# Kernel tuning notes

Hardware: AMD Instinct MI355X
Metric: run time of the kernel (lower is better)

## Reference

```python
import jax, jax.numpy as jnp
import numpy as np
import math

B, T, D = 8, 512, 512
H_HEADS, DQ, DV = 8, 64, 64
N_LAYERS, D_HID = 6, 2048
VOCAB, N_CLASSES = 32000, 5
LN_EPS = 1e-5


def setup_inputs() -> dict:
    key = jax.random.key(0)
    ks = jax.random.split(key, 20)
    s = 0.02
    x = jax.random.randint(ks[0], (B, T), 0, VOCAB - 1)
    emb = jax.random.normal(ks[1], (VOCAB, D), jnp.float32) * s
    emb = emb.at[VOCAB - 1].set(0.0)  # padding_idx row is zero
    # per-layer params stacked on leading N axis; weights stored [in, out]
    Wq = jax.random.normal(ks[2], (N_LAYERS, D, H_HEADS * DQ), jnp.float32) * s
    bq = jnp.zeros((N_LAYERS, H_HEADS * DQ), jnp.float32)
    Wk = jax.random.normal(ks[3], (N_LAYERS, D, H_HEADS * DQ), jnp.float32) * s
    bk = jnp.zeros((N_LAYERS, H_HEADS * DQ), jnp.float32)
    Wv = jax.random.normal(ks[4], (N_LAYERS, D, H_HEADS * DV), jnp.float32) * s
    bv = jnp.zeros((N_LAYERS, H_HEADS * DV), jnp.float32)
    Wo = jax.random.normal(ks[5], (N_LAYERS, H_HEADS * DV, D), jnp.float32) * s
    bo = jnp.zeros((N_LAYERS, D), jnp.float32)
    gamma = jnp.ones((N_LAYERS, D), jnp.float32)
    beta = jnp.zeros((N_LAYERS, D), jnp.float32)
    W1 = jax.random.normal(ks[6], (N_LAYERS, D, D_HID), jnp.float32) * s
    b1 = jnp.zeros((N_LAYERS, D_HID), jnp.float32)
    W2 = jax.random.normal(ks[7], (N_LAYERS, D_HID, D), jnp.float32) * s
    b2 = jnp.zeros((N_LAYERS, D), jnp.float32)
    Wout = jax.random.normal(ks[8], (D * T, N_CLASSES), jnp.float32) * s
    bout = jnp.zeros((N_CLASSES,), jnp.float32)
    return dict(x=x, stage=0, emb=emb, Wq=Wq, bq=bq, Wk=Wk, bk=bk, Wv=Wv, bv=bv,
                Wo=Wo, bo=bo, gamma=gamma, beta=beta, W1=W1, b1=b1, W2=W2, b2=b2,
                Wout=Wout, bout=bout)


def _sinusoidal_pe(t, d):
    pos = jnp.arange(t, dtype=jnp.float32)[:, None]              # [T,1]
    inv = jnp.exp(jnp.arange(0, d, 2, dtype=jnp.float32) * (-math.log(10000.0) / d))
    ang = pos * inv[None, :]                                     # [T, D/2]
    pe = jnp.ones((t, d), jnp.float32)
    pe = pe.at[:, 0::2].set(jnp.sin(ang)).at[:, 1::2].set(jnp.cos(ang))
    return pe


def _layer_norm(x, g, b):
    mu = jnp.mean(x, -1, keepdims=True)
    var = jnp.mean((x - mu) ** 2, -1, keepdims=True)
    return g * (x - mu) * jax.lax.rsqrt(var + LN_EPS) + b


def _attn(x, wq, bq_, wk, bk_, wv, bv_, wo, bo_):
    b, t, _ = x.shape
    q = (x @ wq + bq_).reshape(b, t, H_HEADS, DQ).transpose(0, 2, 1, 3)  # [B,h,T,dq]
    k = (x @ wk + bk_).reshape(b, t, H_HEADS, DQ).transpose(0, 2, 1, 3)
    v = (x @ wv + bv_).reshape(b, t, H_HEADS, DV).transpose(0, 2, 1, 3)
    score = jnp.einsum('bhtd,bhsd->bhts', q, k)  # NOTE: no 1/sqrt(d) scaling, per source
    a = jax.nn.softmax(score, axis=-1)
    o = jnp.einsum('bhts,bhsv->bhtv', a, v)
    o = o.transpose(0, 2, 1, 3).reshape(b, t, H_HEADS * DV)
    return o @ wo + bo_


def reference(x, stage, emb, Wq, bq, Wk, bk, Wv, bv, Wo, bo, gamma, beta, W1, b1, W2, b2, Wout, bout):
    h = emb[x]                                   # [B,T,D]
    h = h + _sinusoidal_pe(h.shape[1], h.shape[2])[None]
    for i in range(N_LAYERS):
        res = h
        a = _attn(h, Wq[i], bq[i], Wk[i], bk[i], Wv[i], bv[i], Wo[i], bo[i])
        h = _layer_norm(a + res, gamma[i], beta[i])
        res = h
        f = jax.nn.relu(h @ W1[i] + b1[i]) @ W2[i] + b2[i]
        h = _layer_norm(f + res, gamma[i], beta[i])  # same LN params reused, per source
    out = h.reshape(h.shape[0], -1) @ Wout + bout
    return out
```

## Files before the change

### kernel.cpp

```cpp
#include <hip/hip_runtime.h>
#include <hip/hip_bf16.h>


typedef _Float16 f16_t;
typedef _Float16 f16x8 __attribute__((ext_vector_type(8)));
typedef _Float16 f16x4 __attribute__((ext_vector_type(4)));
typedef _Float16 f16x2 __attribute__((ext_vector_type(2)));
typedef float    f32x4 __attribute__((ext_vector_type(4)));

#define LSTR 3145728LL

__device__ __forceinline__ void gl_lds16(const f16_t* g, f16_t* l) {
    __builtin_amdgcn_global_load_lds(
        (const __attribute__((address_space(1))) unsigned int*)g,
        (__attribute__((address_space(3))) unsigned int*)l, 16, 0, 0);
}

template<int BM, int BN, int BK, int WR, int WC, int OUTF16, int RELU, int VOUT>
__global__ void __launch_bounds__(256)
gemm_kernel(const f16_t* __restrict__ A, const f16_t* __restrict__ B,
            const float* __restrict__ bias, void* __restrict__ Cout,
            f16_t* __restrict__ vt,
            int M, int N, int K, int lda, int ldb, int ldc, int zmod,
            long long sAhi, long long sAlo, long long sBhi, long long sBlo,
            long long sChi, long long sClo)
{
    constexpr int WMT = BM / WR;
    constexpr int WNT = BN / WC;
    constexpr int MR  = WMT / 16;
    constexpr int NR  = WNT / 16;
    constexpr int KK  = BK / 32;
    constexpr int CPR = BK / 8;
    constexpr int RS  = (BK == 32) ? 1 : 0;
    constexpr int IA  = BM * BK / 2048;
    constexpr int IB  = BN * BK / 2048;
    __shared__ __align__(16) f16_t As[2][BM][BK];
    __shared__ __align__(16) f16_t Bs[2][BN][BK];

    const int tid  = threadIdx.x;
    const int wid  = tid >> 6, lane = tid & 63;
    const int wr   = wid / WC, wc = wid % WC;
    const int z    = blockIdx.z;
    const int zh   = z / zmod, zl = z % zmod;
    const f16_t* Ab = A + (long long)zh * sAhi + (long long)zl * sAlo;
    const f16_t* Bb = B + (long long)zh * sBhi + (long long)zl * sBlo;
    const int m0 = blockIdx.x * BM;
    const int n0 = blockIdx.y * BN;

    f32x4 acc[MR][NR] = {};

    const f16_t* srcA[IA]; const f16_t* srcB[IB];
#pragma unroll
    for (int i = 0; i < IA; ++i) {
        const int c = i * 256 + tid, row = c / CPR;
        const int kch = (c % CPR) ^ ((row >> RS) & (CPR - 1));
        srcA[i] = Ab + (long long)(m0 + row) * lda + kch * 8;
    }
#pragma unroll
    for (int i = 0; i < IB; ++i) {
        const int c = i * 256 + tid, row = c / CPR;
        const int kch = (c % CPR) ^ ((row >> RS) & (CPR - 1));
        srcB[i] = Bb + (long long)(n0 + row) * ldb + kch * 8;
    }
    auto stage = [&](int bf_, int t) {
        const int k0 = t * BK;
#pragma unroll
        for (int i = 0; i < IA; ++i)
            gl_lds16(srcA[i] + k0, &As[bf_][0][0] + (i * 256 + wid * 64) * 8);
#pragma unroll
        for (int i = 0; i < IB; ++i)
            gl_lds16(srcB[i] + k0, &Bs[bf_][0][0] + (i * 256 + wid * 64) * 8);
    };

    const int l15 = lane & 15;
    const int g   = lane >> 4;
    int aoff[MR][KK], boff[NR][KK];
#pragma unroll
    for (int m = 0; m < MR; ++m) {
        const int row = wr * WMT + m * 16 + l15;
        const int swz = ((row >> RS) & (CPR - 1)) << 4;
#pragma unroll
        for (int kk = 0; kk < KK; ++kk)
            aoff[m][kk] = ((row * BK + kk * 32 + g * 8) * 2) ^ swz;
    }
#pragma unroll
    for (int n = 0; n < NR; ++n) {
        const int row = wc * WNT + n * 16 + l15;
        const int swz = ((row >> RS) & (CPR - 1)) << 4;
#pragma unroll
        for (int kk = 0; kk < KK; ++kk)
            boff[n][kk] = ((row * BK + kk * 32 + g * 8) * 2) ^ swz;
    }

    const int NT = K / BK;
    stage(0, 0);
    __syncthreads();

    int buf = 0;
    for (int t = 0; t < NT; ++t) {
        if (t + 1 < NT) stage(buf ^ 1, t + 1);
        const char* Al = (const char*)&As[buf][0][0];
        const char* Bl = (const char*)&Bs[buf][0][0];
        f16x8 af[MR][KK], bfr[NR][KK];
#pragma unroll
        for (int m = 0; m < MR; ++m)
#pragma unroll
            for (int kk = 0; kk < KK; ++kk) af[m][kk] = *(const f16x8*)(Al + aoff[m][kk]);
#pragma unroll
        for (int n = 0; n < NR; ++n)
#pragma unroll
            for (int kk = 0; kk < KK; ++kk) bfr[n][kk] = *(const f16x8*)(Bl + boff[n][kk]);
#pragma unroll
        for (int kk = 0; kk < KK; ++kk)
#pragma unroll
            for (int m = 0; m < MR; ++m)
#pragma unroll
                for (int n = 0; n < NR; ++n)
                    acc[m][n] = __builtin_amdgcn_mfma_f32_16x16x32_f16(af[m][kk], bfr[n][kk], acc[m][n], 0, 0, 0);
        __syncthreads();
        buf ^= 1;
    }

    const long long cOff = (long long)zh * sChi + (long long)zl * sClo;
    const int rbase = (lane >> 4) * 4;
#pragma unroll
    for (int m = 0; m < MR; ++m) {
        const int row = m0 + wr * WMT + m * 16 + rbase;
#pragma unroll
        for (int n = 0; n < NR; ++n) {
            const int col = n0 + wc * WNT + n * 16 + l15;
            const float bb = bias ? bias[col] : 0.0f;
            if (VOUT && col >= 1024) {
                const int hh = (col - 1024) >> 6, dv = (col - 1024) & 63;
                const int bb_ = row >> 9, t0 = row & 511;
                f16x4 v4;
#pragma unroll
                for (int r = 0; r < 4; ++r) v4[r] = (f16_t)(acc[m][n][r] + bb);
                *(f16x4*)&vt[((long long)((bb_ * 8 + hh) * 64 + dv)) * 512 + t0] = v4;
            } else {
#pragma unroll
                for (int r = 0; r < 4; ++r) {
                    float v = acc[m][n][r] + bb;
                    if (RELU) v = fmaxf(v, 0.0f);
                    const long long idx = cOff + (long long)(row + r) * ldc + col;
                    if (OUTF16) ((f16_t*)Cout)[idx] = (f16_t)v;
                    else        ((float*)Cout)[idx] = v;
                }
            }
        }
    }
}

__global__ void __launch_bounds__(256)
attn_flash_kernel(const f16_t* __restrict__ qkv, const f16_t* __restrict__ Vt,
                  f16_t* __restrict__ ao)
{
    __shared__ __align__(16) f16_t Ks[512 * 64];
    __shared__ __align__(16) f16_t Qs[64 * 64];
    __shared__ __align__(16) f16_t Ps[4][16 * 64];
    const int tid = threadIdx.x, wid = tid >> 6, lane = tid & 63;
    const int l15 = lane & 15, g = lane >> 4;
    const int z = blockIdx.y, b = z >> 3, hh = z & 7;
    const int q0 = blockIdx.x * 64;
    const f16_t* Kbase = qkv + (long long)b * 512 * 1536 + 512 + hh * 64;
    const f16_t* Qbase = qkv + (long long)(b * 512 + q0) * 1536 + hh * 64;
    const f16_t* Vbase = Vt + (long long)z * 32768;

#pragma unroll
    for (int i = 0; i < 16; ++i) {
        const int c = i * 256 + tid, t = c >> 3, j = c & 7;
        gl_lds16(Kbase + (long long)t * 1536 + ((j ^ (t & 7)) << 3), Ks + c * 8);
    }
#pragma unroll
    for (int i = 0; i < 2; ++i) {
        const int c = i * 256 + tid, t = c >> 3, j = c & 7;
        gl_lds16(Qbase + (long long)t * 1536 + ((j ^ (t & 7)) << 3), Qs + c * 8);
    }
    __syncthreads();

    const int q = wid * 16 + l15;
    f16x8 qf[2];
#pragma unroll
    for (int k = 0; k < 2; ++k)
        qf[k] = *(const f16x8*)(Qs + q * 64 + (((k * 4 + g) ^ (l15 & 7)) << 3));

    f32x4 ov[4] = {};
    float m_run = -1e30f, l_run = 0.0f;
    f16_t* Pw = &Ps[wid][0];

    for (int ck = 0; ck < 8; ++ck) {
        const int kc0 = ck * 64;
        f16x8 vf[4][2];
#pragma unroll
        for (int n = 0; n < 4; ++n)
#pragma unroll
            for (int k = 0; k < 2; ++k)
                vf[n][k] = *(const f16x8*)(Vbase + (n * 16 + l15) * 512 + kc0 + k * 32 + g * 8);
        f32x4 s[4] = {};
        __builtin_amdgcn_s_setprio(1);
#pragma unroll
        for (int k = 0; k < 2; ++k)
#pragma unroll
            for (int m = 0; m < 4; ++m) {
                const int key = kc0 + m * 16 + l15;
                const f16x8 a = *(const f16x8*)(Ks + key * 64 + (((k * 4 + g) ^ (key & 7)) << 3));
                s[m] = __builtin_amdgcn_mfma_f32_16x16x32_f16(a, qf[k], s[m], 0, 0, 0);
            }
        __builtin_amdgcn_s_setprio(0);
        float cmax = -1e30f;
#pragma unroll
        for (int m = 0; m < 4; ++m)
#pragma unroll
            for (int r = 0; r < 4; ++r) cmax = fmaxf(cmax, s[m][r]);
        cmax = fmaxf(cmax, __shfl_xor(cmax, 16, 64));
        cmax = fmaxf(cmax, __shfl_xor(cmax, 32, 64));
        const float mnew = fmaxf(m_run, cmax);
        const float corr = __expf(m_run - mnew);
        float csum = 0.0f;
#pragma unroll
        for (int m = 0; m < 4; ++m) {
            f16x4 p4;
#pragma unroll
            for (int r = 0; r < 4; ++r) {
                const float pe = __expf(s[m][r] - mnew);
                csum += pe;
                p4[r] = (f16_t)pe;
            }
            *(f16x4*)(Pw + l15 * 64 + ((((m * 2 + (g >> 1)) ^ (l15 & 7))) << 3) + ((g & 1) << 2)) = p4;
        }
        csum += __shfl_xor(csum, 16, 64);
        csum += __shfl_xor(csum, 32, 64);
        l_run = l_run * corr + csum;
        m_run = mnew;
        float cr[4];
#pragma unroll
        for (int r = 0; r < 4; ++r) cr[r] = __shfl(corr, g * 4 + r, 64);
#pragma unroll
        for (int n = 0; n < 4; ++n)
#pragma unroll
            for (int r = 0; r < 4; ++r) ov[n][r] *= cr[r];
#pragma unroll
        for (int k = 0; k < 2; ++k) {
            const f16x8 pf = *(const f16x8*)(Pw + l15 * 64 + (((k * 4 + g) ^ (l15 & 7)) << 3));
            __builtin_amdgcn_s_setprio(1);
#pragma unroll
            for (int n = 0; n < 4; ++n)
                ov[n] = __builtin_amdgcn_mfma_f32_16x16x32_f16(pf, vf[n][k], ov[n], 0, 0, 0);
            __builtin_amdgcn_s_setprio(0);
        }
    }

    const float inv = 1.0f / l_run;
    float ir[4];
#pragma unroll
    for (int r = 0; r < 4; ++r) ir[r] = __shfl(inv, g * 4 + r, 64);
#pragma unroll
    for (int n = 0; n < 4; ++n)
#pragma unroll
        for (int r = 0; r < 4; ++r) {
            const long long row = b * 512 + q0 + wid * 16 + g * 4 + r;
            ao[row * 512 + hh * 64 + n * 16 + l15] = (f16_t)(ov[n][r] * ir[r]);
        }
}

__global__ void __launch_bounds__(256)
setup_kernel(const float* __restrict__ Wq, const float* __restrict__ Wk,
             const float* __restrict__ Wv, const float* __restrict__ Wo,
             const float* __restrict__ W1, const float* __restrict__ W2,
             f16_t* __restrict__ wT,
             const int* __restrict__ xt, const float* __restrict__ emb,
             f16_t* __restrict__ hb,
             const float* __restrict__ bq, const float* __restrict__ bk,
             const float* __restrict__ bv, float* __restrict__ qkvb)
{
    __shared__ float tile[64][65];
    const int blk = blockIdx.x;
    const int tid = threadIdx.x;
    if (blk < 4608) {
        const int layer = blk / 768;
        const int r     = blk % 768;
        const float* src; f16_t* dst; int R, C, tt;
        if (r < 256) {
            const int mat = r >> 6; tt = r & 63; R = 512; C = 512;
            const float* s4 = (mat == 0) ? Wq : (mat == 1) ? Wk : (mat == 2) ? Wv : Wo;
            src = s4 + (long long)layer * 262144;
            dst = wT + (long long)layer * LSTR + (long long)mat * 262144;
        } else if (r < 512) {
            tt = r - 256; R = 512; C = 2048;
            src = W1 + (long long)layer * 1048576;
            dst = wT + (long long)layer * LSTR + 1048576;
        } else {
            tt = r - 512; R = 2048; C = 512;
            src = W2 + (long long)layer * 1048576;
            dst = wT + (long long)layer * LSTR + 2097152;
        }
        const int tC = C >> 6;
        const int tr = tt / tC, tc = tt % tC;
        const int r0 = tr * 64, c0 = tc * 64;
        const int tx = tid & 15, ty = tid >> 4;
#pragma unroll
        for (int i = 0; i < 4; ++i)
            *(float4*)&tile[ty + 16 * i][tx * 4] =
                *(const float4*)&src[(long long)(r0 + ty + 16 * i) * C + c0 + tx * 4];
        __syncthreads();
#pragma unroll
        for (int i = 0; i < 4; ++i) {
            f16x4 o;
#pragma unroll
            for (int e = 0; e < 4; ++e) o[e] = (f16_t)tile[tx * 4 + e][ty + 16 * i];
            *(f16x4*)&dst[(long long)(c0 + ty + 16 * i) * R + r0 + tx * 4] = o;
        }
    } else if (blk < 4608 + 4096) {
        const int row = blk - 4608;
        const int t   = row & 511;
        const int tok = xt[row];
#pragma unroll
        for (int s = 0; s < 2; ++s) {
            const int d = tid + s * 256;
            const int i = d >> 1;
            const float inv = expf((float)(2 * i) * (-9.210340371976184f / 512.0f));
            const float ang = (float)t * inv;
            const float pe  = (d & 1) ? cosf(ang) : sinf(ang);
            hb[(long long)row * 512 + d] = (f16_t)(emb[(long long)tok * 512 + d] + pe);
        }
    } else {
        const int i = (blk - 8704) * 256 + tid;
        if (i < 9216) {
            const int l = i / 1536, c = i % 1536;
            float v;
            if (c < 512)       v = bq[l * 512 + c];
            else if (c < 1024) v = bk[l * 512 + c - 512];
            else               v = bv[l * 512 + c - 1024];
            qkvb[i] = v;
        }
    }
}

__global__ void __launch_bounds__(256)
add_ln_kernel(const f16_t* __restrict__ X, int ns, long long sstr,
              const float* __restrict__ bias,
              const float* __restrict__ g, const float* __restrict__ b,
              f16_t* __restrict__ Hf)
{
    const int wid = threadIdx.x >> 6, lane = threadIdx.x & 63;
    const long long row = (long long)blockIdx.x * 4 + wid;
    f16_t* h = Hf + row * 512;
    const int c0 = lane * 8;
    const f16x8 hv = *(const f16x8*)&h[c0];
    float v[8];
#pragma unroll
    for (int e = 0; e < 8; ++e) v[e] = (float)hv[e] + bias[c0 + e];
    for (int s = 0; s < ns; ++s) {
        const f16x8 xv = *(const f16x8*)&X[s * sstr + row * 512 + c0];
#pragma unroll
        for (int e = 0; e < 8; ++e) v[e] += (float)xv[e];
    }
    float sum = 0.0f, sq = 0.0f;
#pragma unroll
    for (int e = 0; e < 8; ++e) { sum += v[e]; sq += v[e] * v[e]; }
#pragma unroll
    for (int o = 1; o < 64; o <<= 1) {
        sum += __shfl_xor(sum, o, 64);
        sq  += __shfl_xor(sq,  o, 64);
    }
    const float mu = sum * (1.0f / 512.0f);
    float var = sq * (1.0f / 512.0f) - mu * mu;
    var = fmaxf(var, 0.0f);
    const float rs = rsqrtf(var + 1e-5f);
    f16x8 o8;
#pragma unroll
    for (int e = 0; e < 8; ++e)
        o8[e] = (f16_t)(g[c0 + e] * (v[e] - mu) * rs + b[c0 + e]);
    *(f16x8*)&h[c0] = o8;
}

__global__ void head_partial_kernel(const f16_t* __restrict__ hb, const float* __restrict__ Wout,
                                    float* __restrict__ partials)
{
    const int blk = blockIdx.x;
    const int b = blk >> 6, chunk = blk & 63;
    const int tid = threadIdx.x;
    const f16_t* hp = hb + (long long)b * 262144 + (long long)chunk * 4096;
    float a0 = 0, a1 = 0, a2 = 0, a3 = 0, a4 = 0;
    for (int it = 0; it < 16; ++it) {
        const int idx = it * 256 + tid;
        const float hv = (float)hp[idx];
        const float* w = Wout + ((long long)chunk * 4096 + idx) * 5;
        a0 += hv * w[0]; a1 += hv * w[1]; a2 += hv * w[2]; a3 += hv * w[3]; a4 += hv * w[4];
    }
#pragma unroll
    for (int o = 32; o > 0; o >>= 1) {
        a0 += __shfl_down(a0, o, 64); a1 += __shfl_down(a1, o, 64); a2 += __shfl_down(a2, o, 64);
        a3 += __shfl_down(a3, o, 64); a4 += __shfl_down(a4, o, 64);
    }
    __shared__ float sm[4][5];
    const int lane = tid & 63, w = tid >> 6;
    if (lane == 0) { sm[w][0] = a0; sm[w][1] = a1; sm[w][2] = a2; sm[w][3] = a3; sm[w][4] = a4; }
    __syncthreads();
    if (tid < 5)
        partials[(long long)blk * 5 + tid] = sm[0][tid] + sm[1][tid] + sm[2][tid] + sm[3][tid];
}

__global__ void head_final_kernel(const float* __restrict__ partials, const float* __restrict__ bout,
                                  float* __restrict__ out)
{
    const int tid = threadIdx.x;
    if (tid >= 40) return;
    const int b = tid / 5, c = tid % 5;
    float s = bout[c];
    const float* p = partials + (long long)b * 64 * 5 + c;
    for (int ck = 0; ck < 64; ++ck) s += p[ck * 5];
    out[tid] = s;
}

extern "C" void kernel_launch(void* const* d_in, const int* in_sizes, int n_in,
                              void* d_out, int out_size, void* d_ws, size_t ws_size,
                              hipStream_t stream)
{
    (void)in_sizes; (void)n_in; (void)out_size; (void)ws_size;
    const int*   x_tok = (const int*)  d_in[0];
    const float* emb   = (const float*)d_in[2];
    const float* Wq    = (const float*)d_in[3];
    const float* bq    = (const float*)d_in[4];
    const float* Wk    = (const float*)d_in[5];
    const float* bk    = (const float*)d_in[6];
    const float* Wv    = (const float*)d_in[7];
    const float* bv    = (const float*)d_in[8];
    const float* Wo    = (const float*)d_in[9];
    const float* bo    = (const float*)d_in[10];
    const float* gma   = (const float*)d_in[11];
    const float* bta   = (const float*)d_in[12];
    const float* W1    = (const float*)d_in[13];
    const float* b1    = (const float*)d_in[14];
    const float* W2    = (const float*)d_in[15];
    const float* b2    = (const float*)d_in[16];
    const float* Wout  = (const float*)d_in[17];
    const float* bout  = (const float*)d_in[18];

    char* ws = (char*)d_ws;
    size_t off = 0;
    auto take = [&](size_t bytes) { char* p = ws + off; off += (bytes + 255) & ~(size_t)255; return p; };
    f16_t* wT    = (f16_t*)take(18874368ULL * 2);
    f16_t* hb    = (f16_t*)take(2097152ULL * 2);
    f16_t* qkv   = (f16_t*)take(6291456ULL * 2);
    f16_t* Vt    = (f16_t*)take(2097152ULL * 2);
    f16_t* ao    = (f16_t*)take(2097152ULL * 2);
    f16_t* f1    = (f16_t*)take(8388608ULL * 2);
    f16_t* t16   = (f16_t*)take(4ULL * 2097152ULL * 2);
    float* qkvb  = (float*)take(9216ULL * 4);
    float* parts = (float*)take(2560ULL * 4);

    setup_kernel<<<dim3(8740), 256, 0, stream>>>(Wq, Wk, Wv, Wo, W1, W2, wT,
                                                 x_tok, emb, hb, bq, bk, bv, qkvb);

    for (int l = 0; l < 6; ++l) {
        const f16_t* wl = wT + (long long)l * LSTR;
        gemm_kernel<64,128,64,2,2,1,0,1><<<dim3(64,12,1),256,0,stream>>>(hb, wl, qkvb + l*1536,
            qkv, Vt, 4096,1536,512, 512,512,1536, 1, 0,0,0,0,0,0);
        attn_flash_kernel<<<dim3(8,64),256,0,stream>>>(qkv, Vt, ao);
        gemm_kernel<64,128,64,2,2,1,0,0><<<dim3(64,4,2),256,0,stream>>>(ao, wl + 786432, nullptr,
            t16, nullptr, 4096,512,256, 512,512,512, 1, 256LL,0LL, 256LL,0LL, 2097152LL,0LL);
        add_ln_kernel<<<dim3(1024),256,0,stream>>>(t16, 2, 2097152LL, bo + l*512,
            gma + l*512, bta + l*512, hb);
        gemm_kernel<128,128,32,2,2,1,1,0><<<dim3(32,16,1),256,0,stream>>>(hb, wl + 1048576, b1 + l*2048,
            f1, nullptr, 4096,2048,512, 512,512,2048, 1, 0,0,0,0,0,0);
        gemm_kernel<128,128,32,2,2,1,0,0><<<dim3(32,4,4),256,0,stream>>>(f1, wl + 2097152, nullptr,
            t16, nullptr, 4096,512,512, 2048,2048,512, 1, 512LL,0LL, 512LL,0LL, 2097152LL,0LL);
        add_ln_kernel<<<dim3(1024),256,0,stream>>>(t16, 4, 2097152LL, b2 + l*512,
            gma + l*512, bta + l*512, hb);
    }

    head_partial_kernel<<<dim3(512),256,0,stream>>>(hb, Wout, parts);
    head_final_kernel  <<<dim3(1),64,0,stream>>>(parts, bout, (float*)d_out);
}
```

Baseline: 561.2 us.

## Double-buffer K tiles in flash attention and load Q directly to registers

Replaces the up-front load of the whole 512-key K block into LDS with a two-buffer pipeline of 128-key chunks, prefetching the next chunk while the current one is used. Q fragments are read straight from global memory instead of being staged through LDS. LDS use drops from about 80KB to about 40KB per block, which could allow more resident blocks and overlaps load latency with MFMA work. It adds a barrier per chunk and uses uncoalesced direct Q loads.

```diff
diff --git a/kernel.cpp b/kernel.cpp
--- a/kernel.cpp
+++ b/kernel.cpp
@@ -155,8 +155,7 @@
 attn_flash_kernel(const f16_t* __restrict__ qkv, const f16_t* __restrict__ Vt,
                   f16_t* __restrict__ ao)
 {
-    __shared__ __align__(16) f16_t Ks[512 * 64];
-    __shared__ __align__(16) f16_t Qs[64 * 64];
+    __shared__ __align__(16) f16_t Ks[2][128 * 64];
     __shared__ __align__(16) f16_t Ps[4][16 * 64];
     const int tid = threadIdx.x, wid = tid >> 6, lane = tid & 63;
     const int l15 = lane & 15, g = lane >> 4;
@@ -166,88 +165,97 @@
     const f16_t* Qbase = qkv + (long long)(b * 512 + q0) * 1536 + hh * 64;
     const f16_t* Vbase = Vt + (long long)z * 32768;
 
-#pragma unroll
-    for (int i = 0; i < 16; ++i) {
-        const int c = i * 256 + tid, t = c >> 3, j = c & 7;
-        gl_lds16(Kbase + (long long)t * 1536 + ((j ^ (t & 7)) << 3), Ks + c * 8);
-    }
-#pragma unroll
-    for (int i = 0; i < 2; ++i) {
-        const int c = i * 256 + tid, t = c >> 3, j = c & 7;
-        gl_lds16(Qbase + (long long)t * 1536 + ((j ^ (t & 7)) << 3), Qs + c * 8);
-    }
-    __syncthreads();
+    auto stageK = [&](int bf_, int c) {
+#pragma unroll
+        for (int i = 0; i < 4; ++i) {
+            const int ci = i * 256 + tid, t = ci >> 3, j = ci & 7;
+            gl_lds16(Kbase + (long long)(c * 128 + t) * 1536 + ((j ^ (t & 7)) << 3),
+                     &Ks[bf_][0] + ci * 8);
+        }
+    };
 
     const int q = wid * 16 + l15;
     f16x8 qf[2];
 #pragma unroll
     for (int k = 0; k < 2; ++k)
-        qf[k] = *(const f16x8*)(Qs + q * 64 + (((k * 4 + g) ^ (l15 & 7)) << 3));
+        qf[k] = *(const f16x8*)(Qbase + (long long)q * 1536 + k * 32 + g * 8);
+
+    stageK(0, 0);
 
     f32x4 ov[4] = {};
     float m_run = -1e30f, l_run = 0.0f;
     f16_t* Pw = &Ps[wid][0];
 
-    for (int ck = 0; ck < 8; ++ck) {
-        const int kc0 = ck * 64;
-        f16x8 vf[4][2];
-#pragma unroll
-        for (int n = 0; n < 4; ++n)
+    __syncthreads();
+
+    int buf = 0;
+    for (int c = 0; c < 4; ++c) {
+        if (c + 1 < 4) stageK(buf ^ 1, c + 1);
+#pragma unroll
+        for (int sub = 0; sub < 2; ++sub) {
+            const int kc0 = c * 128 + sub * 64;
+            f16x8 vf[4][2];
+#pragma unroll
+            for (int n = 0; n < 4; ++n)
+#pragma unroll
+                for (int k = 0; k < 2; ++k)
+                    vf[n][k] = *(const f16x8*)(Vbase + (n * 16 + l15) * 512 + kc0 + k * 32 + g * 8);
+            f32x4 s[4] = {};
+            __builtin_amdgcn_s_setprio(1);
 #pragma unroll
             for (int k = 0; k < 2; ++k)
-                vf[n][k] = *(const f16x8*)(Vbase + (n * 16 + l15) * 512 + kc0 + k * 32 + g * 8);
-        f32x4 s[4] = {};
-        __builtin_amdgcn_s_setprio(1);
-#pragma unroll
-        for (int k = 0; k < 2; ++k)
+#pragma unroll
+                for (int m = 0; m < 4; ++m) {
+                    const int lr = sub * 64 + m * 16 + l15;
+                    const f16x8 a = *(const f16x8*)(&Ks[buf][0] + lr * 64 +
+                                       (((k * 4 + g) ^ (lr & 7)) << 3));
+                    s[m] = __builtin_amdgcn_mfma_f32_16x16x32_f16(a, qf[k], s[m], 0, 0, 0);
+                }
+            __builtin_amdgcn_s_setprio(0);
+            float cmax = -1e30f;
+#pragma unroll
+            for (int m = 0; m < 4; ++m)
+#pragma unroll
+                for (int r = 0; r < 4; ++r) cmax = fmaxf(cmax, s[m][r]);
+            cmax = fmaxf(cmax, __shfl_xor(cmax, 16, 64));
+            cmax = fmaxf(cmax, __shfl_xor(cmax, 32, 64));
+            const float mnew = fmaxf(m_run, cmax);
+            const float corr = __expf(m_run - mnew);
+            float csum = 0.0f;
 #pragma unroll
             for (int m = 0; m < 4; ++m) {
-                const int key = kc0 + m * 16 + l15;
-                const f16x8 a = *(const f16x8*)(Ks + key * 64 + (((k * 4 + g) ^ (key & 7)) << 3));
-                s[m] = __builtin_amdgcn_mfma_f32_16x16x32_f16(a, qf[k], s[m], 0, 0, 0);
+                f16x4 p4;
+#pragma unroll
+                for (int r = 0; r < 4; ++r) {
+                    const float pe = __expf(s[m][r] - mnew);
+                    csum += pe;
+                    p4[r] = (f16_t)pe;
+                }
+                *(f16x4*)(Pw + l15 * 64 + ((((m * 2 + (g >> 1)) ^ (l15 & 7))) << 3) + ((g & 1) << 2)) = p4;
             }
-        __builtin_amdgcn_s_setprio(0);
-        float cmax = -1e30f;
-#pragma unroll
-        for (int m = 0; m < 4; ++m)
-#pragma unroll
-            for (int r = 0; r < 4; ++r) cmax = fmaxf(cmax, s[m][r]);
-        cmax = fmaxf(cmax, __shfl_xor(cmax, 16, 64));
-        cmax = fmaxf(cmax, __shfl_xor(cmax, 32, 64));
-        const float mnew = fmaxf(m_run, cmax);
-        const float corr = __expf(m_run - mnew);
-        float csum = 0.0f;
-#pragma unroll
-        for (int m = 0; m < 4; ++m) {
-            f16x4 p4;
-#pragma unroll
-            for (int r = 0; r < 4; ++r) {
-                const float pe = __expf(s[m][r] - mnew);
-                csum += pe;
-                p4[r] = (f16_t)pe;
+            csum += __shfl_xor(csum, 16, 64);
+            csum += __shfl_xor(csum, 32, 64);
+            l_run = l_run * corr + csum;
+            m_run = mnew;
+            float cr[4];
+#pragma unroll
+            for (int r = 0; r < 4; ++r) cr[r] = __shfl(corr, g * 4 + r, 64);
+#pragma unroll
+            for (int n = 0; n < 4; ++n)
+#pragma unroll
+                for (int r = 0; r < 4; ++r) ov[n][r] *= cr[r];
+#pragma unroll
+            for (int k = 0; k < 2; ++k) {
+                const f16x8 pf = *(const f16x8*)(Pw + l15 * 64 + (((k * 4 + g) ^ (l15 & 7)) << 3));
+                __builtin_amdgcn_s_setprio(1);
+#pragma unroll
+                for (int n = 0; n < 4; ++n)
+                    ov[n] = __builtin_amdgcn_mfma_f32_16x16x32_f16(pf, vf[n][k], ov[n], 0, 0, 0);
+                __builtin_amdgcn_s_setprio(0);
             }
-            *(f16x4*)(Pw + l15 * 64 + ((((m * 2 + (g >> 1)) ^ (l15 & 7))) << 3) + ((g & 1) << 2)) = p4;
-        }
-        csum += __shfl_xor(csum, 16, 64);
-        csum += __shfl_xor(csum, 32, 64);
-        l_run = l_run * corr + csum;
-        m_run = mnew;
-        float cr[4];
-#pragma unroll
-        for (int r = 0; r < 4; ++r) cr[r] = __shfl(corr, g * 4 + r, 64);
-#pragma unroll
-        for (int n = 0; n < 4; ++n)
-#pragma unroll
-            for (int r = 0; r < 4; ++r) ov[n][r] *= cr[r];
-#pragma unroll
-        for (int k = 0; k < 2; ++k) {
-            const f16x8 pf = *(const f16x8*)(Pw + l15 * 64 + (((k * 4 + g) ^ (l15 & 7)) << 3));
-            __builtin_amdgcn_s_setprio(1);
-#pragma unroll
-            for (int n = 0; n < 4; ++n)
-                ov[n] = __builtin_amdgcn_mfma_f32_16x16x32_f16(pf, vf[n][k], ov[n], 0, 0, 0);
-            __builtin_amdgcn_s_setprio(0);
-        }
+        }
+        __syncthreads();
+        buf ^= 1;
     }
 
     const float inv = 1.0f / l_run;
```

Result: no change. 557.7 us (-0.6%).
